# Performance work log

Measured on AMD Instinct MI355X. Metric: run time of the kernel, lower is better.

Reference implementation:

```python
import jax, jax.numpy as jnp
import numpy as np

N, D, E = 100000, 32, 1600000
EH, NH = 32, 16
TAU = 0.1


def setup_inputs() -> dict:
    key = jax.random.key(0)
    ks = jax.random.split(key, 12)
    x = jax.random.normal(ks[0], (N, D), dtype=jnp.float32)
    edge_index = jax.random.randint(ks[1], (2, E), 0, N, dtype=jnp.int32)
    hsd = jax.random.normal(ks[2], (N,), dtype=jnp.float32)
    s_e1 = 1.0 / np.sqrt(D + 2)
    s_e2 = 1.0 / np.sqrt(EH)
    s_n2 = 1.0 / np.sqrt(NH)
    We1 = jax.random.uniform(ks[3], (D + 2, EH), jnp.float32, -s_e1, s_e1)
    be1 = jax.random.uniform(ks[4], (EH,), jnp.float32, -s_e1, s_e1)
    We2 = jax.random.uniform(ks[5], (EH, 1), jnp.float32, -s_e2, s_e2)
    be2 = jax.random.uniform(ks[6], (1,), jnp.float32, -s_e2, s_e2)
    Wn1 = jax.random.uniform(ks[7], (1, NH), jnp.float32, -1.0, 1.0)
    bn1 = jax.random.uniform(ks[8], (NH,), jnp.float32, -1.0, 1.0)
    Wn2 = jax.random.uniform(ks[9], (NH, 1), jnp.float32, -s_n2, s_n2)
    bn2 = jax.random.uniform(ks[10], (1,), jnp.float32, -s_n2, s_n2)
    return {"x": x, "hsd": hsd, "We1": We1, "be1": be1, "We2": We2, "be2": be2,
            "Wn1": Wn1, "bn1": bn1, "Wn2": Wn2, "bn2": bn2, "edge_index": edge_index}


def reference(x, hsd, We1, be1, We2, be2, Wn1, bn1, Wn2, bn2, edge_index):
    row, col = edge_index[0], edge_index[1]
    n = x.shape[0]
    # normalized HSD (torch.std is unbiased, ddof=1)
    hsd_norm = (hsd - hsd.mean()) / (jnp.std(hsd, ddof=1) + 1e-8)
    # edge MLP input: [hsd_u, hsd_v, |x_u - x_v|]  -> (E, D+2)
    diff_abs = jnp.abs(x[row] - x[col])
    edge_in = jnp.concatenate([hsd_norm[row][:, None], hsd_norm[col][:, None], diff_abs], axis=1)
    h = jax.nn.relu(edge_in @ We1 + be1)
    e_uv = (h @ We2 + be2)[:, 0]  # (E,)
    # segment softmax over destination (col)
    logits = e_uv / TAU
    seg_max = jax.ops.segment_max(logits, col, num_segments=n)
    seg_max = jnp.where(jnp.isfinite(seg_max), seg_max, 0.0)
    ex = jnp.exp(logits - seg_max[col])
    denom = jax.ops.segment_sum(ex, col, num_segments=n)
    alpha_uv = (ex / (denom[col] + 1e-16))[:, None]  # (E,1)
    # node-level gate
    gh = jax.nn.relu(hsd_norm[:, None] @ Wn1 + bn1)
    alpha_bar = jax.nn.sigmoid(gh @ Wn2 + bn2)  # (N,1)
    # degree normalization
    ones = jnp.ones(row.shape[0], dtype=x.dtype)
    src_deg = jnp.sqrt(jnp.clip(jax.ops.segment_sum(ones, row, num_segments=n), 1.0))
    dst_deg = jnp.sqrt(jnp.clip(jax.ops.segment_sum(ones, col, num_segments=n), 1.0))
    edge_w = 1.0 / (src_deg[row] * dst_deg[col])
    low_pass = jax.ops.segment_sum(edge_w[:, None] * x[row], col, num_segments=n)
    high_pass = jax.ops.segment_sum(alpha_uv * (x[col] - x[row]), col, num_segments=n)
    return (1.0 - alpha_bar) * low_pass + alpha_bar * high_pass
```

## Files before the change

kernel.cpp:

```cpp
#include <hip/hip_runtime.h>

#define D_FEAT 32
#define IN_DIM 34
#define EHID 32
#define NHID 16
#define INV_TAU 10.0f
#define SCAN_CHUNK 1024
#define EPB 256
#define XSH 40
#define TILE 8192
#define BSH 7
#define NBIN 128
#define BMASK 127
#define CAP 3072

__device__ __forceinline__ unsigned enc_f32(float f) {
    unsigned b = __float_as_uint(f);
    return (b & 0x80000000u) ? ~b : (b | 0x80000000u);
}
__device__ __forceinline__ float dec_f32(unsigned e) {
    unsigned b = (e & 0x80000000u) ? (e & 0x7fffffffu) : ~e;
    return __uint_as_float(b);
}
__device__ __forceinline__ unsigned short f2bf(float f) {
    unsigned u = __float_as_uint(f);
    u += 0x7fffu + ((u >> 16) & 1u);
    return (unsigned short)(u >> 16);
}

__global__ __launch_bounds__(256) void k1_hsd_stats(const float* __restrict__ hsd,
                                                    double* __restrict__ stats, int N) {
    double s = 0.0, s2 = 0.0;
    for (int i = blockIdx.x * 256 + threadIdx.x; i < N; i += gridDim.x * 256) {
        double v = (double)hsd[i];
        s += v; s2 += v * v;
    }
    for (int off = 32; off > 0; off >>= 1) {
        s  += __shfl_down(s,  off, 64);
        s2 += __shfl_down(s2, off, 64);
    }
    __shared__ double ls[4], ls2[4];
    int wid = threadIdx.x >> 6, lid = threadIdx.x & 63;
    if (lid == 0) { ls[wid] = s; ls2[wid] = s2; }
    __syncthreads();
    if (threadIdx.x == 0) {
        double ts = 0.0, t2 = 0.0;
        for (int w = 0; w < 4; ++w) { ts += ls[w]; t2 += ls2[w]; }
        atomicAdd(stats, ts);
        atomicAdd(stats + 1, t2);
    }
}

__global__ __launch_bounds__(256) void k2_node_prep(const float* __restrict__ hsd,
                                                    const double* __restrict__ stats,
                                                    const float* __restrict__ Wn1,
                                                    const float* __restrict__ bn1,
                                                    const float* __restrict__ Wn2,
                                                    const float* __restrict__ bn2,
                                                    float* __restrict__ hsd_norm,
                                                    float* __restrict__ alpha_bar, int N) {
    int n = blockIdx.x * 256 + threadIdx.x;
    if (n >= N) return;
    double sum = stats[0], sumsq = stats[1];
    double mean = sum / (double)N;
    double var  = (sumsq - sum * sum / (double)N) / (double)(N - 1);
    float stdv  = (float)sqrt(var);
    float hn = (hsd[n] - (float)mean) / (stdv + 1e-8f);
    hsd_norm[n] = hn;
    float acc = bn2[0];
#pragma unroll
    for (int k = 0; k < NHID; ++k)
        acc += fmaxf(fmaf(hn, Wn1[k], bn1[k]), 0.0f) * Wn2[k];
    alpha_bar[n] = 1.0f / (1.0f + __expf(-acc));
}

__global__ __launch_bounds__(256) void s1_hist(const int* __restrict__ ei,
                                               int* __restrict__ hist,
                                               int E, int NB, int T, int M) {
    __shared__ int hv[1024], hu[1024];
    int t = threadIdx.x;
    for (int b = t; b < 1024; b += 256) { hv[b] = 0; hu[b] = 0; }
    __syncthreads();
    int base = blockIdx.x * TILE;
    for (int i = t; i < TILE; i += 256) {
        int e = base + i;
        if (e < E) {
            int u = ei[e], v = ei[E + e];
            atomicAdd(&hv[v >> BSH], 1);
            atomicAdd(&hu[u >> BSH], 1);
        }
    }
    __syncthreads();
    for (int b = t; b < NB; b += 256) {
        hist[b * T + blockIdx.x] = hv[b];
        hist[M + b * T + blockIdx.x] = hu[b];
    }
}

__global__ __launch_bounds__(256) void scan_k1(const int* __restrict__ cnt,
                                               int* __restrict__ out,
                                               int* __restrict__ partials, int N) {
    __shared__ int lds[256];
    int base = blockIdx.x * SCAN_CHUNK;
    int t = threadIdx.x;
    int v[4]; int loc = 0;
#pragma unroll
    for (int k = 0; k < 4; ++k) {
        int idx = base + t * 4 + k;
        v[k] = (idx < N) ? cnt[idx] : 0;
        loc += v[k];
    }
    lds[t] = loc; __syncthreads();
    for (int off = 1; off < 256; off <<= 1) {
        int a = (t >= off) ? lds[t - off] : 0;
        __syncthreads();
        lds[t] += a;
        __syncthreads();
    }
    int run = (t > 0) ? lds[t - 1] : 0;
    if (t == 255) partials[blockIdx.x] = lds[255];
#pragma unroll
    for (int k = 0; k < 4; ++k) {
        run += v[k];
        int idx = base + t * 4 + k;
        if (idx < N) out[idx + 1] = run;
    }
    if (blockIdx.x == 0 && t == 0) out[0] = 0;
}

__global__ __launch_bounds__(256) void scan_k2(int* __restrict__ partials, int B) {
    __shared__ int lds[256];
    int t = threadIdx.x;
    int v[4]; int loc = 0;
#pragma unroll
    for (int k = 0; k < 4; ++k) {
        int idx = t * 4 + k;
        v[k] = (idx < B) ? partials[idx] : 0;
        loc += v[k];
    }
    lds[t] = loc; __syncthreads();
    for (int off = 1; off < 256; off <<= 1) {
        int a = (t >= off) ? lds[t - off] : 0;
        __syncthreads();
        lds[t] += a;
        __syncthreads();
    }
    int run = (t > 0) ? lds[t - 1] : 0;
#pragma unroll
    for (int k = 0; k < 4; ++k) {
        int idx = t * 4 + k;
        if (idx < B) { partials[idx] = run; run += v[k]; }
    }
}

__global__ __launch_bounds__(256) void scan_k3(int* __restrict__ out,
                                               const int* __restrict__ partials, int N) {
    int i = blockIdx.x * 256 + threadIdx.x;
    if (i >= N) return;
    out[i + 1] += partials[i / SCAN_CHUNK];
}

__global__ __launch_bounds__(256) void s2_scatter(const int* __restrict__ ei,
                                                  const int* __restrict__ scanAll,
                                                  int2* __restrict__ coarse,
                                                  int* __restrict__ coarseU,
                                                  int E, int NB, int T, int M) {
    __shared__ int curV[1024], curU[1024];
    int t = threadIdx.x;
    for (int b = t; b < NB; b += 256) {
        curV[b] = scanAll[b * T + blockIdx.x];
        curU[b] = scanAll[M + b * T + blockIdx.x] - E;
    }
    __syncthreads();
    int base = blockIdx.x * TILE;
    for (int i = t; i < TILE; i += 256) {
        int e = base + i;
        if (e < E) {
            int u = ei[e], v = ei[E + e];
            int pv = atomicAdd(&curV[v >> BSH], 1);
            coarse[pv] = make_int2(u, v);
            int pu = atomicAdd(&curU[u >> BSH], 1);
            coarseU[pu] = u;
        }
    }
}

__global__ __launch_bounds__(256) void s3b_srccnt(const int* __restrict__ coarseU,
                                                  const int* __restrict__ scanAll,
                                                  float* __restrict__ inv_ssrc,
                                                  int N, int E, int NB, int T, int M) {
    __shared__ int cnt[NBIN];
    int t = threadIdx.x;
    int bin = blockIdx.x;
    int start = scanAll[M + bin * T] - E;
    int endv  = scanAll[M + (bin + 1) * T] - E;
    if (t < NBIN) cnt[t] = 0;
    __syncthreads();
    for (int i = start + t; i < endv; i += 256) atomicAdd(&cnt[coarseU[i] & BMASK], 1);
    __syncthreads();
    int vglob = (bin << BSH) + t;
    if (t < NBIN && vglob < N) inv_ssrc[vglob] = rsqrtf(fmaxf((float)cnt[t], 1.0f));
}

__global__ __launch_bounds__(256) void k3c_mlp(const float* __restrict__ x,
                                               const float* __restrict__ hsd_norm,
                                               const float* __restrict__ We1,
                                               const float* __restrict__ be1,
                                               const float* __restrict__ We2,
                                               const float* __restrict__ be2,
                                               const int2* __restrict__ esorted,
                                               float* __restrict__ logit, int E) {
    __shared__ unsigned short sxu[EPB * XSH];
    int t = threadIdx.x;
    int base = blockIdx.x * EPB;

    int q = t & 7;
#pragma unroll
    for (int k = 0; k < 8; ++k) {
        int s = (t >> 3) + 32 * k;
        int e = base + s;
        int u = esorted[(e < E) ? e : (E - 1)].x;
        float4 val = *(const float4*)(x + (size_t)u * D_FEAT + 4 * q);
        ushort4 pk;
        pk.x = f2bf(val.x); pk.y = f2bf(val.y);
        pk.z = f2bf(val.z); pk.w = f2bf(val.w);
        *(ushort4*)(sxu + s * XSH + 4 * q) = pk;
    }
    __syncthreads();

    int e = base + t;
    if (e >= E) return;
    int2 uv = esorted[e];
    int u = uv.x, v = uv.y;

    float in0 = hsd_norm[u];
    float in1 = hsd_norm[v];

    float diff[D_FEAT];
    const float4* xv = (const float4*)(x + (size_t)v * D_FEAT);
    const unsigned* p = (const unsigned*)(sxu + (size_t)t * XSH);
#pragma unroll
    for (int qq = 0; qq < 8; ++qq) {
        float4 b = xv[qq];
        unsigned ua = p[2 * qq];
        unsigned ub = p[2 * qq + 1];
        diff[4 * qq + 0] = fabsf(__uint_as_float(ua << 16) - b.x);
        diff[4 * qq + 1] = fabsf(__uint_as_float(ua & 0xFFFF0000u) - b.y);
        diff[4 * qq + 2] = fabsf(__uint_as_float(ub << 16) - b.z);
        diff[4 * qq + 3] = fabsf(__uint_as_float(ub & 0xFFFF0000u) - b.w);
    }

    float h[EHID];
#pragma unroll
    for (int j = 0; j < EHID; ++j)
        h[j] = fmaf(in0, We1[j], fmaf(in1, We1[EHID + j], be1[j]));
#pragma unroll
    for (int i = 0; i < D_FEAT; ++i) {
        float a = diff[i];
#pragma unroll
        for (int j = 0; j < EHID; ++j)
            h[j] = fmaf(a, We1[(i + 2) * EHID + j], h[j]);
    }
    float acc = be2[0];
#pragma unroll
    for (int j = 0; j < EHID; ++j)
        acc += fmaxf(h[j], 0.0f) * We2[j];

    logit[e] = acc * INV_TAU;
}

__global__ __launch_bounds__(512) void k6a_tab(const int2* __restrict__ coarse,
                                               const float* __restrict__ logit,
                                               const int* __restrict__ scanAll,
                                               const float* __restrict__ inv_ssrc,
                                               const float* __restrict__ alpha_bar,
                                               int* __restrict__ usrc,
                                               float* __restrict__ coefG,
                                               int* __restrict__ dst_off,
                                               float* __restrict__ selfc,
                                               int N, int E, int NB, int T) {
    __shared__ int      su[CAP];
    __shared__ float    slg[CAP];
    __shared__ int      cnt[NBIN];
    __shared__ unsigned mEnc[NBIN];
    __shared__ float    den[NBIN], cA[NBIN], cB[NBIN];
    __shared__ int      base_[NBIN], cur_[NBIN];

    int t = threadIdx.x;
    int bin = blockIdx.x;
    int start = scanAll[bin * T];
    int n = scanAll[(bin + 1) * T] - start;
    if (n > CAP) n = CAP;

    if (t < NBIN) { cnt[t] = 0; mEnc[t] = 0u; den[t] = 0.0f; }
    __syncthreads();

    for (int i = t; i < n; i += 512) {
        int2 c = coarse[start + i];
        float lgv = logit[start + i];
        int vl = c.y & BMASK;
        su[i] = c.x | (vl << 17);
        slg[i] = lgv;
        atomicAdd(&cnt[vl], 1);
        atomicMax(&mEnc[vl], enc_f32(lgv));
    }
    __syncthreads();

    for (int i = t; i < n; i += 512) {
        int vl = su[i] >> 17;
        atomicAdd(&den[vl], __expf(slg[i] - dec_f32(mEnc[vl])));
    }
    __syncthreads();

    for (int off = 1; off < NBIN; off <<= 1) {
        int a = 0;
        if (t < NBIN && t >= off) a = cnt[t - off];
        __syncthreads();
        if (t < NBIN) cnt[t] += a;
        __syncthreads();
    }
    if (t < NBIN) {
        int b0 = (t > 0) ? cnt[t - 1] : 0;
        base_[t] = b0; cur_[t] = b0;
        int vg = (bin << BSH) + t;
        if (vg < N) {
            float ab = alpha_bar[vg];
            float d = den[t];
            float inv_den = 1.0f / (d + 1e-16f);
            int deg = cnt[t] - b0;
            cA[t] = -ab * inv_den;
            cB[t] = (1.0f - ab) * rsqrtf(fmaxf((float)deg, 1.0f));
            dst_off[vg] = start + b0;
            selfc[vg] = ab * (d * inv_den);
        }
    }
    if (bin == 0 && t == 0) dst_off[N] = E;
    __syncthreads();

    for (int i = t; i < n; i += 512) {
        int up = su[i];
        int vl = up >> 17;
        int u = up & 0x1FFFF;
        int p = start + atomicAdd(&cur_[vl], 1);
        float coef = fmaf(cA[vl], __expf(slg[i] - dec_f32(mEnc[vl])), cB[vl] * inv_ssrc[u]);
        usrc[p] = u;
        coefG[p] = coef;
    }
}

__global__ __launch_bounds__(256) void k7_gather(const float* __restrict__ x,
                                                 const int* __restrict__ dst_off,
                                                 const int* __restrict__ usrc,
                                                 const float* __restrict__ coefG,
                                                 const float* __restrict__ selfc,
                                                 float* __restrict__ out, int N) {
    int v = blockIdx.x * 8 + (threadIdx.x >> 5);
    if (v >= N) return;
    int l = threadIdx.x & 31;

    int beg = dst_off[v], end = dst_off[v + 1];

    float acc = 0.0f;
    int j = beg;
    for (; j + 3 < end; j += 4) {
        int u0 = usrc[j], u1 = usrc[j + 1], u2 = usrc[j + 2], u3 = usrc[j + 3];
        float c0 = coefG[j], c1 = coefG[j + 1], c2 = coefG[j + 2], c3 = coefG[j + 3];
        float x0 = x[(size_t)u0 * D_FEAT + l];
        float x1 = x[(size_t)u1 * D_FEAT + l];
        float x2 = x[(size_t)u2 * D_FEAT + l];
        float x3 = x[(size_t)u3 * D_FEAT + l];
        acc = fmaf(c0, x0, acc);
        acc = fmaf(c1, x1, acc);
        acc = fmaf(c2, x2, acc);
        acc = fmaf(c3, x3, acc);
    }
    for (; j < end; ++j)
        acc = fmaf(coefG[j], x[(size_t)usrc[j] * D_FEAT + l], acc);

    out[(size_t)v * D_FEAT + l] = fmaf(selfc[v], x[(size_t)v * D_FEAT + l], acc);
}

extern "C" void kernel_launch(void* const* d_in, const int* in_sizes, int n_in,
                              void* d_out, int out_size, void* d_ws, size_t ws_size,
                              hipStream_t stream) {
    const float* x    = (const float*)d_in[0];
    const float* hsd  = (const float*)d_in[1];
    const float* We1  = (const float*)d_in[2];
    const float* be1  = (const float*)d_in[3];
    const float* We2  = (const float*)d_in[4];
    const float* be2  = (const float*)d_in[5];
    const float* Wn1  = (const float*)d_in[6];
    const float* bn1  = (const float*)d_in[7];
    const float* Wn2  = (const float*)d_in[8];
    const float* bn2  = (const float*)d_in[9];
    const int*   ei   = (const int*)d_in[10];
    float* out = (float*)d_out;

    const int N = in_sizes[1];
    const int E = in_sizes[10] / 2;
    const int NB = (N + NBIN - 1) >> BSH;
    const int T  = (E + TILE - 1) / TILE;
    const int M  = NB * T;
    const int M2 = 2 * M;

    char* ws = (char*)d_ws;
    size_t o = 0;
    auto alloc = [&](size_t bytes) { size_t r = o; o += (bytes + 255) & ~(size_t)255; return r; };
    double* stats     = (double*)(ws + alloc(16));
    float*  inv_ssrc  = (float*)(ws + alloc((size_t)4 * N));
    float*  hsd_norm  = (float*)(ws + alloc((size_t)4 * N));
    float*  alpha_bar = (float*)(ws + alloc((size_t)4 * N));
    float*  selfc     = (float*)(ws + alloc((size_t)4 * N));
    int*    dst_off   = (int*)(ws + alloc((size_t)4 * (N + 1)));
    int*    partials  = (int*)(ws + alloc(4096));
    int*    bufH      = (int*)(ws + alloc((size_t)4 * M2));
    int*    bufS      = (int*)(ws + alloc((size_t)4 * (M2 + 1)));
    int2*   coarse    = (int2*)(ws + alloc((size_t)8 * E));
    int*    coarseU   = (int*)(ws + alloc((size_t)4 * E));
    float*  logit     = (float*)coarseU;
    int*    usrc      = (int*)(ws + alloc((size_t)4 * E));
    float*  coefG     = (float*)(ws + alloc((size_t)4 * E));

    hipMemsetAsync(d_ws, 0, 256, stream);

    k1_hsd_stats<<<256, 256, 0, stream>>>(hsd, stats, N);
    k2_node_prep<<<(N + 255) / 256, 256, 0, stream>>>(hsd, stats, Wn1, bn1, Wn2, bn2,
                                                      hsd_norm, alpha_bar, N);

    s1_hist<<<T, 256, 0, stream>>>(ei, bufH, E, NB, T, M);

    int Bs = (M2 + SCAN_CHUNK - 1) / SCAN_CHUNK;
    scan_k1<<<Bs, 256, 0, stream>>>(bufH, bufS, partials, M2);
    scan_k2<<<1, 256, 0, stream>>>(partials, Bs);
    scan_k3<<<(M2 + 255) / 256, 256, 0, stream>>>(bufS, partials, M2);

    s2_scatter<<<T, 256, 0, stream>>>(ei, bufS, coarse, coarseU, E, NB, T, M);
    s3b_srccnt<<<NB, 256, 0, stream>>>(coarseU, bufS, inv_ssrc, N, E, NB, T, M);
    k3c_mlp<<<(E + EPB - 1) / EPB, 256, 0, stream>>>(x, hsd_norm, We1, be1, We2, be2,
                                                     coarse, logit, E);
    k6a_tab<<<NB, 512, 0, stream>>>(coarse, logit, bufS, inv_ssrc, alpha_bar,
                                    usrc, coefG, dst_off, selfc, N, E, NB, T);
    k7_gather<<<(N + 7) / 8, 256, 0, stream>>>(x, dst_off, usrc, coefG, selfc, out, N);
}
```

Baseline: 301.6 us.

## Compute edge MLP with bf16 MFMA and gather from bf16-packed features

The edge MLP first layer moves from per-thread scalar FMAs to bf16 MFMA 16x16x32 instructions. Edge |x_u-x_v| diffs and the hsd inputs are staged in LDS as bf16, and the weights are pre-swizzled into B fragments. The final aggregation gathers from a bf16-packed copy of x, written into the reused coarse buffer by a new pack kernel, which halves gather bytes. The cost is lower precision in the hidden activations and the output, plus one extra small kernel launch.

```diff
diff --git a/kernel.cpp b/kernel.cpp
--- a/kernel.cpp
+++ b/kernel.cpp
@@ -1,19 +1,21 @@
 #include <hip/hip_runtime.h>
 
 #define D_FEAT 32
-#define IN_DIM 34
 #define EHID 32
 #define NHID 16
 #define INV_TAU 10.0f
 #define SCAN_CHUNK 1024
 #define EPB 256
-#define XSH 40
+#define SDS 40
 #define TILE 8192
 #define BSH 7
 #define NBIN 128
 #define BMASK 127
 #define CAP 3072
 
+typedef __attribute__((ext_vector_type(8))) short short8v;
+typedef __attribute__((ext_vector_type(4))) float f32x4;
+
 __device__ __forceinline__ unsigned enc_f32(float f) {
     unsigned b = __float_as_uint(f);
     return (b & 0x80000000u) ? ~b : (b | 0x80000000u);
@@ -27,6 +29,8 @@
     u += 0x7fffu + ((u >> 16) & 1u);
     return (unsigned short)(u >> 16);
 }
+__device__ __forceinline__ float bflo(unsigned u) { return __uint_as_float(u << 16); }
+__device__ __forceinline__ float bfhi(unsigned u) { return __uint_as_float(u & 0xFFFF0000u); }
 
 __global__ __launch_bounds__(256) void k1_hsd_stats(const float* __restrict__ hsd,
                                                     double* __restrict__ stats, int N) {
@@ -202,7 +206,7 @@
     if (t < NBIN && vglob < N) inv_ssrc[vglob] = rsqrtf(fmaxf((float)cnt[t], 1.0f));
 }
 
-__global__ __launch_bounds__(256) void k3c_mlp(const float* __restrict__ x,
+__global__ __launch_bounds__(256) void k3d_mlp(const float* __restrict__ x,
                                                const float* __restrict__ hsd_norm,
                                                const float* __restrict__ We1,
                                                const float* __restrict__ be1,
@@ -210,63 +214,85 @@
                                                const float* __restrict__ be2,
                                                const int2* __restrict__ esorted,
                                                float* __restrict__ logit, int E) {
-    __shared__ unsigned short sxu[EPB * XSH];
-    int t = threadIdx.x;
+    __shared__ unsigned short sdiff[EPB * SDS];
+    __shared__ unsigned short sB[4 * 64 * 8];
+
+    int t = threadIdx.x;
+    {
+        int f = t >> 6, l = t & 63;
+        int c = f >> 1, hh = f & 1;
+        int col = hh * 16 + (l & 15);
+        int k0 = c * 32 + (l >> 4) * 8;
+        unsigned short vals[8];
+#pragma unroll
+        for (int b = 0; b < 8; ++b) {
+            int k = k0 + b;
+            int row = (k < 32) ? (k + 2) : (k == 32 ? 0 : (k == 33 ? 1 : -1));
+            float w = (row >= 0) ? We1[row * EHID + col] : 0.0f;
+            vals[b] = f2bf(w);
+        }
+        *(uint4*)&sB[(f * 64 + l) * 8] = *(const uint4*)vals;
+    }
+
     int base = blockIdx.x * EPB;
-
     int q = t & 7;
 #pragma unroll
     for (int k = 0; k < 8; ++k) {
         int s = (t >> 3) + 32 * k;
         int e = base + s;
-        int u = esorted[(e < E) ? e : (E - 1)].x;
-        float4 val = *(const float4*)(x + (size_t)u * D_FEAT + 4 * q);
+        int ec = (e < E) ? e : (E - 1);
+        int2 uv = esorted[ec];
+        float4 a = *(const float4*)(x + (size_t)uv.x * D_FEAT + 4 * q);
+        float4 b = *(const float4*)(x + (size_t)uv.y * D_FEAT + 4 * q);
         ushort4 pk;
-        pk.x = f2bf(val.x); pk.y = f2bf(val.y);
-        pk.z = f2bf(val.z); pk.w = f2bf(val.w);
-        *(ushort4*)(sxu + s * XSH + 4 * q) = pk;
-    }
-    __syncthreads();
-
-    int e = base + t;
-    if (e >= E) return;
-    int2 uv = esorted[e];
-    int u = uv.x, v = uv.y;
-
-    float in0 = hsd_norm[u];
-    float in1 = hsd_norm[v];
-
-    float diff[D_FEAT];
-    const float4* xv = (const float4*)(x + (size_t)v * D_FEAT);
-    const unsigned* p = (const unsigned*)(sxu + (size_t)t * XSH);
-#pragma unroll
-    for (int qq = 0; qq < 8; ++qq) {
-        float4 b = xv[qq];
-        unsigned ua = p[2 * qq];
-        unsigned ub = p[2 * qq + 1];
-        diff[4 * qq + 0] = fabsf(__uint_as_float(ua << 16) - b.x);
-        diff[4 * qq + 1] = fabsf(__uint_as_float(ua & 0xFFFF0000u) - b.y);
-        diff[4 * qq + 2] = fabsf(__uint_as_float(ub << 16) - b.z);
-        diff[4 * qq + 3] = fabsf(__uint_as_float(ub & 0xFFFF0000u) - b.w);
-    }
-
-    float h[EHID];
-#pragma unroll
-    for (int j = 0; j < EHID; ++j)
-        h[j] = fmaf(in0, We1[j], fmaf(in1, We1[EHID + j], be1[j]));
-#pragma unroll
-    for (int i = 0; i < D_FEAT; ++i) {
-        float a = diff[i];
-#pragma unroll
-        for (int j = 0; j < EHID; ++j)
-            h[j] = fmaf(a, We1[(i + 2) * EHID + j], h[j]);
-    }
-    float acc = be2[0];
-#pragma unroll
-    for (int j = 0; j < EHID; ++j)
-        acc += fmaxf(h[j], 0.0f) * We2[j];
-
-    logit[e] = acc * INV_TAU;
+        pk.x = f2bf(fabsf(a.x - b.x));
+        pk.y = f2bf(fabsf(a.y - b.y));
+        pk.z = f2bf(fabsf(a.z - b.z));
+        pk.w = f2bf(fabsf(a.w - b.w));
+        *(ushort4*)&sdiff[s * SDS + 4 * q] = pk;
+        if (q == 0) {
+            uint4 z;
+            z.x = (unsigned)f2bf(hsd_norm[uv.x]) | ((unsigned)f2bf(hsd_norm[uv.y]) << 16);
+            z.y = 0u; z.z = 0u; z.w = 0u;
+            *(uint4*)&sdiff[s * SDS + 32] = z;
+        }
+    }
+    __syncthreads();
+
+    int l = t & 63, w = t >> 6;
+    short8v B00 = *(const short8v*)&sB[(0 * 64 + l) * 8];
+    short8v B01 = *(const short8v*)&sB[(1 * 64 + l) * 8];
+    short8v B10 = *(const short8v*)&sB[(2 * 64 + l) * 8];
+    short8v B11 = *(const short8v*)&sB[(3 * 64 + l) * 8];
+    float blo = be1[l & 15], bhi = be1[16 + (l & 15)];
+    float w2lo = We2[l & 15], w2hi = We2[16 + (l & 15)];
+    float b2 = be2[0];
+    int wbase = base + w * 64;
+
+#pragma unroll
+    for (int g = 0; g < 4; ++g) {
+        int row = w * 64 / 1;
+        row = g * 16 + (l & 15) + w * 64;
+        const short8v a0 = *(const short8v*)&sdiff[row * SDS + (l >> 4) * 8];
+        short8v a1 = (short8v)(short)0;
+        if (l < 16) a1 = *(const short8v*)&sdiff[row * SDS + 32];
+        f32x4 c0 = {blo, blo, blo, blo};
+        f32x4 c1 = {bhi, bhi, bhi, bhi};
+        c0 = __builtin_amdgcn_mfma_f32_16x16x32_bf16(a0, B00, c0, 0, 0, 0);
+        c0 = __builtin_amdgcn_mfma_f32_16x16x32_bf16(a1, B10, c0, 0, 0, 0);
+        c1 = __builtin_amdgcn_mfma_f32_16x16x32_bf16(a0, B01, c1, 0, 0, 0);
+        c1 = __builtin_amdgcn_mfma_f32_16x16x32_bf16(a1, B11, c1, 0, 0, 0);
+#pragma unroll
+        for (int r = 0; r < 4; ++r) {
+            float vsum = fmaxf(c0[r], 0.0f) * w2lo + fmaxf(c1[r], 0.0f) * w2hi;
+            vsum += __shfl_xor(vsum, 1, 64);
+            vsum += __shfl_xor(vsum, 2, 64);
+            vsum += __shfl_xor(vsum, 4, 64);
+            vsum += __shfl_xor(vsum, 8, 64);
+            int eo = wbase + g * 16 + (l >> 4) * 4 + r;
+            if ((l & 15) == r && eo < E) logit[eo] = (vsum + b2) * INV_TAU;
+        }
+    }
 }
 
 __global__ __launch_bounds__(512) void k6a_tab(const int2* __restrict__ coarse,
@@ -348,36 +374,51 @@
     }
 }
 
-__global__ __launch_bounds__(256) void k7_gather(const float* __restrict__ x,
+__global__ __launch_bounds__(256) void kx_pack(const float* __restrict__ x,
+                                               unsigned* __restrict__ xbf, int n2) {
+    int i = blockIdx.x * 256 + threadIdx.x;
+    if (i >= n2) return;
+    float2 f = *(const float2*)(x + 2 * (size_t)i);
+    xbf[i] = (unsigned)f2bf(f.x) | ((unsigned)f2bf(f.y) << 16);
+}
+
+__global__ __launch_bounds__(256) void k7_gather(const unsigned* __restrict__ xbf,
                                                  const int* __restrict__ dst_off,
                                                  const int* __restrict__ usrc,
                                                  const float* __restrict__ coefG,
                                                  const float* __restrict__ selfc,
                                                  float* __restrict__ out, int N) {
-    int v = blockIdx.x * 8 + (threadIdx.x >> 5);
+    int v = blockIdx.x * 16 + (threadIdx.x >> 4);
     if (v >= N) return;
-    int l = threadIdx.x & 31;
+    int l = threadIdx.x & 15;
 
     int beg = dst_off[v], end = dst_off[v + 1];
 
-    float acc = 0.0f;
+    float a0 = 0.0f, a1 = 0.0f;
     int j = beg;
     for (; j + 3 < end; j += 4) {
         int u0 = usrc[j], u1 = usrc[j + 1], u2 = usrc[j + 2], u3 = usrc[j + 3];
         float c0 = coefG[j], c1 = coefG[j + 1], c2 = coefG[j + 2], c3 = coefG[j + 3];
-        float x0 = x[(size_t)u0 * D_FEAT + l];
-        float x1 = x[(size_t)u1 * D_FEAT + l];
-        float x2 = x[(size_t)u2 * D_FEAT + l];
-        float x3 = x[(size_t)u3 * D_FEAT + l];
-        acc = fmaf(c0, x0, acc);
-        acc = fmaf(c1, x1, acc);
-        acc = fmaf(c2, x2, acc);
-        acc = fmaf(c3, x3, acc);
-    }
-    for (; j < end; ++j)
-        acc = fmaf(coefG[j], x[(size_t)usrc[j] * D_FEAT + l], acc);
-
-    out[(size_t)v * D_FEAT + l] = fmaf(selfc[v], x[(size_t)v * D_FEAT + l], acc);
+        unsigned q0 = xbf[(size_t)u0 * 16 + l];
+        unsigned q1 = xbf[(size_t)u1 * 16 + l];
+        unsigned q2 = xbf[(size_t)u2 * 16 + l];
+        unsigned q3 = xbf[(size_t)u3 * 16 + l];
+        a0 = fmaf(c0, bflo(q0), a0); a1 = fmaf(c0, bfhi(q0), a1);
+        a0 = fmaf(c1, bflo(q1), a0); a1 = fmaf(c1, bfhi(q1), a1);
+        a0 = fmaf(c2, bflo(q2), a0); a1 = fmaf(c2, bfhi(q2), a1);
+        a0 = fmaf(c3, bflo(q3), a0); a1 = fmaf(c3, bfhi(q3), a1);
+    }
+    for (; j < end; ++j) {
+        unsigned q0 = xbf[(size_t)usrc[j] * 16 + l];
+        float c0 = coefG[j];
+        a0 = fmaf(c0, bflo(q0), a0); a1 = fmaf(c0, bfhi(q0), a1);
+    }
+    float sc = selfc[v];
+    unsigned qv = xbf[(size_t)v * 16 + l];
+    a0 = fmaf(sc, bflo(qv), a0);
+    a1 = fmaf(sc, bfhi(qv), a1);
+    float2 r; r.x = a0; r.y = a1;
+    *(float2*)(out + (size_t)v * D_FEAT + 2 * l) = r;
 }
 
 extern "C" void kernel_launch(void* const* d_in, const int* in_sizes, int n_in,
@@ -420,6 +461,7 @@
     float*  logit     = (float*)coarseU;
     int*    usrc      = (int*)(ws + alloc((size_t)4 * E));
     float*  coefG     = (float*)(ws + alloc((size_t)4 * E));
+    unsigned* xbf     = (unsigned*)coarse;
 
     hipMemsetAsync(d_ws, 0, 256, stream);
 
@@ -436,9 +478,10 @@
 
     s2_scatter<<<T, 256, 0, stream>>>(ei, bufS, coarse, coarseU, E, NB, T, M);
     s3b_srccnt<<<NB, 256, 0, stream>>>(coarseU, bufS, inv_ssrc, N, E, NB, T, M);
-    k3c_mlp<<<(E + EPB - 1) / EPB, 256, 0, stream>>>(x, hsd_norm, We1, be1, We2, be2,
+    k3d_mlp<<<(E + EPB - 1) / EPB, 256, 0, stream>>>(x, hsd_norm, We1, be1, We2, be2,
                                                      coarse, logit, E);
     k6a_tab<<<NB, 512, 0, stream>>>(coarse, logit, bufS, inv_ssrc, alpha_bar,
                                     usrc, coefG, dst_off, selfc, N, E, NB, T);
-    k7_gather<<<(N + 7) / 8, 256, 0, stream>>>(x, dst_off, usrc, coefG, selfc, out, N);
-}
+    kx_pack<<<(N * (D_FEAT / 2) + 255) / 256, 256, 0, stream>>>(x, xbf, N * (D_FEAT / 2));
+    k7_gather<<<(N + 15) / 16, 256, 0, stream>>>(xbf, dst_off, usrc, coefG, selfc, out, N);
+}
```

New measurement: 294.5 us. 2.4% less time.
